# Optimization experiments

Measured on AMD Instinct MI355X. Metric: run time of the kernel, lower is better.

## Reference

```python
import jax, jax.numpy as jnp
import numpy as np

D_MODEL = 768
NUM_HEADS = 12
D_K = D_MODEL // NUM_HEADS
SCALE = float(np.sqrt(D_K))


def setup_inputs() -> dict:
    key = jax.random.key(0)
    ks = jax.random.split(key, 9)
    B, S, D = 2, 2048, D_MODEL
    std = 1.0 / np.sqrt(D)
    x = jax.random.normal(ks[0], (B, S, D), dtype=jnp.float32)
    attention_mask = jnp.ones((B, S), dtype=jnp.int32)
    # Linear params: weight [out, in] (torch convention), bias [out]
    Wq = jax.random.normal(ks[1], (D, D), dtype=jnp.float32) * std
    bq = jax.random.normal(ks[2], (D,), dtype=jnp.float32) * 0.01
    Wk = jax.random.normal(ks[3], (D, D), dtype=jnp.float32) * std
    bk = jax.random.normal(ks[4], (D,), dtype=jnp.float32) * 0.01
    Wv = jax.random.normal(ks[5], (D, D), dtype=jnp.float32) * std
    bv = jax.random.normal(ks[6], (D,), dtype=jnp.float32) * 0.01
    Wo = jax.random.normal(ks[7], (D, D), dtype=jnp.float32) * std
    bo = jax.random.normal(ks[8], (D,), dtype=jnp.float32) * 0.01
    return {"x": x, "attention_mask": attention_mask,
            "Wq": Wq, "bq": bq, "Wk": Wk, "bk": bk,
            "Wv": Wv, "bv": bv, "Wo": Wo, "bo": bo}


def reference(x, attention_mask, Wq, bq, Wk, bk, Wv, bv, Wo, bo):
    B, S, D = x.shape
    H, Dk = NUM_HEADS, D_K
    # QKV projections (torch Linear: x @ W.T + b)
    q = (x @ Wq.T + bq).reshape(B, S, H, Dk).transpose(0, 2, 1, 3)  # [B,H,S,Dk]
    k = (x @ Wk.T + bk).reshape(B, S, H, Dk).transpose(0, 2, 1, 3)
    v = (x @ Wv.T + bv).reshape(B, S, H, Dk).transpose(0, 2, 1, 3)
    scores = jnp.einsum('bhqd,bhkd->bhqk', q, k) / SCALE  # [B,H,S,S]
    mask = attention_mask[:, None, None, :]  # [B,1,1,S]
    scores = jnp.where(mask == 0, jnp.float32(-jnp.inf), scores)
    attn = jax.nn.softmax(scores, axis=-1)
    # dropout is identity in eval mode
    ctx = jnp.einsum('bhqk,bhkd->bhqd', attn, v)  # [B,H,S,Dk]
    ctx = ctx.transpose(0, 2, 1, 3).reshape(B, S, D)
    return ctx @ Wo.T + bo
```

## Files before the change

### kernel.cpp

```cpp
#include <hip/hip_runtime.h>
#include <stdint.h>

#define NHEAD 12
#define DKH   64
#define BB    2
#define SS    2048
#define DMOD  768
#define MTOT  (BB*SS)
#define NCHUNK 2
#define CHS   (SS/NCHUNK)
#define QBLK  128
#define NT    (CHS/64)

typedef __attribute__((ext_vector_type(8)))  _Float16 half8;
typedef __attribute__((ext_vector_type(4)))  _Float16 half4;
typedef __attribute__((ext_vector_type(2)))  __fp16   fp16x2;
typedef __attribute__((ext_vector_type(4)))  float    f32x4;
typedef __attribute__((ext_vector_type(16))) float    f32x16;

typedef __attribute__((address_space(1))) const void gv_t;
typedef __attribute__((address_space(3))) void       lv_t;

__device__ inline float fexp2(float x) { return __builtin_amdgcn_exp2f(x); }
__device__ inline int pk2(float a, float b) {
    union { fp16x2 h; int i; } u;
    u.h = __builtin_amdgcn_cvt_pkrtz(a, b);
    return u.i;
}

__global__ void k_cvtall(const float* __restrict__ x,
                         const float* __restrict__ w0, const float* __restrict__ w1,
                         const float* __restrict__ w2, const float* __restrict__ w3,
                         _Float16* __restrict__ xb,
                         _Float16* __restrict__ o0, _Float16* __restrict__ o1,
                         _Float16* __restrict__ o2, _Float16* __restrict__ o3) {
    const float* in; _Float16* out; int base;
    int blk = blockIdx.x;
    if (blk < 3072)      { in = x;  out = xb; base = blk; }
    else if (blk < 3648) { in = w0; out = o0; base = blk - 3072; }
    else if (blk < 4224) { in = w1; out = o1; base = blk - 3648; }
    else if (blk < 4800) { in = w2; out = o2; base = blk - 4224; }
    else                 { in = w3; out = o3; base = blk - 4800; }
    int i = (base * 256 + threadIdx.x) * 4;
    float4 v = *(const float4*)(in + i);
    half4 o;
    o.x = (_Float16)v.x; o.y = (_Float16)v.y; o.z = (_Float16)v.z; o.w = (_Float16)v.w;
    *(half4*)(out + i) = o;
}

template<int MODE>
__global__ __launch_bounds__(256, 2) void k_gemm(
    const _Float16* __restrict__ A, const _Float16* __restrict__ Bm,
    const float* __restrict__ bias0, const float* __restrict__ bias1, const float* __restrict__ bias2,
    float* __restrict__ outF,
    _Float16* __restrict__ Qd, _Float16* __restrict__ Kd, _Float16* __restrict__ Vtd,
    int K, int Ncols)
{
    __shared__ _Float16 As[128 * 64];
    __shared__ _Float16 Bs[128 * 64];
    const int tid = threadIdx.x;
    const int w = tid >> 6, l = tid & 63, lr = l & 15, lg = l >> 4;
    const int bm = blockIdx.y * 128, bn = blockIdx.x * 128;
    const int wm = (w >> 1) * 64, wn = (w & 1) * 64;
    f32x4 acc[4][4] = {};

    for (int k0 = 0; k0 < K; k0 += 64) {
        __syncthreads();
#pragma unroll
        for (int i = 0; i < 4; ++i) {
            int o  = w * 4096 + i * 1024 + l * 16;
            int lo = o ^ (((o >> 7) & 7) << 4);
            int row = lo >> 7;
            int colb = lo & 127;
            __builtin_amdgcn_global_load_lds(
                (gv_t*)((const char*)A + ((size_t)(bm + row) * K + k0) * 2 + colb),
                (lv_t*)((char*)As + w * 4096 + i * 1024), 16, 0, 0);
            __builtin_amdgcn_global_load_lds(
                (gv_t*)((const char*)Bm + ((size_t)(bn + row) * K + k0) * 2 + colb),
                (lv_t*)((char*)Bs + w * 4096 + i * 1024), 16, 0, 0);
        }
        __syncthreads();
#pragma unroll
        for (int kk = 0; kk < 2; ++kk) {
            half8 af[4], bf[4];
#pragma unroll
            for (int f = 0; f < 4; ++f) {
                int ob = ((wm + f * 16 + lr) * 128 + kk * 64 + lg * 16) ^ ((lr & 7) << 4);
                af[f] = *(const half8*)((const char*)As + ob);
                int ob2 = ((wn + f * 16 + lr) * 128 + kk * 64 + lg * 16) ^ ((lr & 7) << 4);
                bf[f] = *(const half8*)((const char*)Bs + ob2);
            }
            __builtin_amdgcn_s_setprio(1);
#pragma unroll
            for (int fm = 0; fm < 4; ++fm)
#pragma unroll
                for (int fn = 0; fn < 4; ++fn)
                    acc[fm][fn] = __builtin_amdgcn_mfma_f32_16x16x32_f16(af[fm], bf[fn], acc[fm][fn], 0, 0, 0);
            __builtin_amdgcn_s_setprio(0);
        }
    }

#pragma unroll
    for (int fm = 0; fm < 4; ++fm) {
#pragma unroll
        for (int fn = 0; fn < 4; ++fn) {
            int n = bn + wn + fn * 16 + lr;
            if (MODE == 0) {
                float bia = bias0[n];
#pragma unroll
                for (int j = 0; j < 4; ++j) {
                    int m = bm + wm + fm * 16 + lg * 4 + j;
                    outF[(size_t)m * Ncols + n] = acc[fm][fn][j] + bia;
                }
            } else {
                int qkv = n / 768, nn = n - qkv * 768;
                const float* bp = (qkv == 0) ? bias0 : (qkv == 1 ? bias1 : bias2);
                float bia = bp[nn];
                int h = nn >> 6, dk = nn & 63;
                int m0 = bm + wm + fm * 16 + lg * 4;
                int b = m0 >> 11;
                int s0 = m0 & 2047;
                size_t head = (size_t)b * NHEAD + h;
                if (qkv == 2) {
                    half4 pk;
#pragma unroll
                    for (int j = 0; j < 4; ++j) pk[j] = (_Float16)(acc[fm][fn][j] + bia);
                    *(half4*)(Vtd + (head * DKH + dk) * SS + s0) = pk;
                } else {
                    _Float16* dst = (qkv == 0) ? Qd : Kd;
                    float qsc = (qkv == 0) ? 0.18033688011f : 1.0f;
#pragma unroll
                    for (int j = 0; j < 4; ++j)
                        dst[(head * SS + (s0 + j)) * DKH + dk] = (_Float16)((acc[fm][fn][j] + bia) * qsc);
                }
            }
        }
    }
}

__global__ __launch_bounds__(256, 3) void k_attn(
    const _Float16* __restrict__ Qd, const _Float16* __restrict__ Kd,
    const _Float16* __restrict__ Vtd, const int* __restrict__ mask,
    _Float16* __restrict__ Opart, float* __restrict__ Mpart, float* __restrict__ Lpart)
{
    __shared__ _Float16 Ks[2 * 64 * 64];
    __shared__ _Float16 Vs[2 * 64 * 64];
    const int tid = threadIdx.x, w = tid >> 6, l = tid & 63;
    const int lq = l & 31, lhi = l >> 5;
    const int head  = blockIdx.x;
    const int qt    = blockIdx.y;
    const int chunk = blockIdx.z;
    const int b = head / NHEAD;
    const char* Qh = (const char*)(Qd + (size_t)head * SS * DKH);
    const char* Kh = (const char*)(Kd + (size_t)head * SS * DKH) + (size_t)chunk * CHS * 128;
    const char* Vh = (const char*)(Vtd + (size_t)head * DKH * SS);
    const int vcb = chunk * CHS * 2;

    const int q = qt * QBLK + w * 32 + lq;
    half8 qf[4];
#pragma unroll
    for (int kd = 0; kd < 4; ++kd)
        qf[kd] = *(const half8*)(Qh + ((size_t)q * 64 + kd * 16 + lhi * 8) * 2);

    f32x16 accO[2] = {};
    float m = -__builtin_inff(), lsum = 0.f;

    auto STAGE = [&](int kt2, int buf) {
#pragma unroll
        for (int i = 0; i < 2; ++i) {
            int o  = w * 2048 + i * 1024 + l * 16;
            int lo = o ^ (((o >> 7) & 7) << 4);
            __builtin_amdgcn_global_load_lds(
                (gv_t*)(Kh + (size_t)kt2 * 8192 + lo),
                (lv_t*)((char*)Ks + buf * 8192 + w * 2048 + i * 1024), 16, 0, 0);
            int dv = lo >> 7, inner = lo & 127;
            __builtin_amdgcn_global_load_lds(
                (gv_t*)(Vh + (size_t)dv * 4096 + vcb + kt2 * 128 + inner),
                (lv_t*)((char*)Vs + buf * 8192 + w * 2048 + i * 1024), 16, 0, 0);
        }
    };

    STAGE(0, 0);
    int cur = 0;

    for (int kt = 0; kt < NT; ++kt) {
        __syncthreads();
        if (kt < NT - 1) STAGE(kt + 1, cur ^ 1);
        int mv = mask[b * SS + chunk * CHS + kt * 64 + l];
        unsigned long long bal = __ballot(mv != 0);
        const char* kb = (const char*)Ks + cur * 8192;
        const char* vb = (const char*)Vs + cur * 8192;

        f32x16 s0 = {}, s1 = {};
#pragma unroll
        for (int kd = 0; kd < 4; ++kd) {
            int col = kd * 32 + lhi * 16;
            int ob0 = (lq * 128 + col) ^ ((lq & 7) << 4);
            half8 kf0 = *(const half8*)(kb + ob0);
            s0 = __builtin_amdgcn_mfma_f32_32x32x16_f16(kf0, qf[kd], s0, 0, 0, 0);
            int ob1 = ((32 + lq) * 128 + col) ^ ((lq & 7) << 4);
            half8 kf1 = *(const half8*)(kb + ob1);
            s1 = __builtin_amdgcn_mfma_f32_32x32x16_f16(kf1, qf[kd], s1, 0, 0, 0);
        }

        if (bal != ~0ull) {
#pragma unroll
            for (int r = 0; r < 16; ++r) {
                int kv0 = (r & 3) + 8 * (r >> 2) + 4 * lhi;
                if (!((bal >> kv0) & 1))        s0[r] = -__builtin_inff();
                if (!((bal >> (kv0 + 32)) & 1)) s1[r] = -__builtin_inff();
            }
        }

        float t[16];
#pragma unroll
        for (int i = 0; i < 16; ++i) t[i] = fmaxf(s0[i], s1[i]);
#pragma unroll
        for (int i = 0; i < 8; ++i) t[i] = fmaxf(t[i], t[i + 8]);
#pragma unroll
        for (int i = 0; i < 4; ++i) t[i] = fmaxf(t[i], t[i + 4]);
        t[0] = fmaxf(fmaxf(t[0], t[2]), fmaxf(t[1], t[3]));
        float pmax = fmaxf(t[0], __shfl_xor(t[0], 32, 64));

        if (!__all(pmax <= m + 3.0f)) {
            float mnew = fmaxf(m, pmax);
            float f = fexp2(m - mnew);
            m = mnew; lsum *= f;
            accO[0] *= f; accO[1] *= f;
        }
        float mex = fmaxf(m, -1e30f);

#pragma unroll
        for (int i = 0; i < 16; ++i) { s0[i] = fexp2(s0[i] - mex); s1[i] = fexp2(s1[i] - mex); }
#pragma unroll
        for (int i = 0; i < 16; ++i) t[i] = s0[i] + s1[i];
#pragma unroll
        for (int i = 0; i < 8; ++i) t[i] = t[i] + t[i + 8];
#pragma unroll
        for (int i = 0; i < 4; ++i) t[i] = t[i] + t[i + 4];
        t[0] = (t[0] + t[2]) + (t[1] + t[3]);
        lsum += t[0] + __shfl_xor(t[0], 32, 64);

        union PF { int w[4]; half8 h; } pf[4];
        {
            int W[8];
#pragma unroll
            for (int mm = 0; mm < 8; ++mm) W[mm] = pk2(s0[2 * mm], s0[2 * mm + 1]);
            asm("v_permlane32_swap_b32 %0, %1" : "+v"(W[0]), "+v"(W[2]));
            asm("v_permlane32_swap_b32 %0, %1" : "+v"(W[1]), "+v"(W[3]));
            asm("v_permlane32_swap_b32 %0, %1" : "+v"(W[4]), "+v"(W[6]));
            asm("v_permlane32_swap_b32 %0, %1" : "+v"(W[5]), "+v"(W[7]));
            pf[0].w[0] = W[0]; pf[0].w[1] = W[1]; pf[0].w[2] = W[2]; pf[0].w[3] = W[3];
            pf[1].w[0] = W[4]; pf[1].w[1] = W[5]; pf[1].w[2] = W[6]; pf[1].w[3] = W[7];
#pragma unroll
            for (int mm = 0; mm < 8; ++mm) W[mm] = pk2(s1[2 * mm], s1[2 * mm + 1]);
            asm("v_permlane32_swap_b32 %0, %1" : "+v"(W[0]), "+v"(W[2]));
            asm("v_permlane32_swap_b32 %0, %1" : "+v"(W[1]), "+v"(W[3]));
            asm("v_permlane32_swap_b32 %0, %1" : "+v"(W[4]), "+v"(W[6]));
            asm("v_permlane32_swap_b32 %0, %1" : "+v"(W[5]), "+v"(W[7]));
            pf[2].w[0] = W[0]; pf[2].w[1] = W[1]; pf[2].w[2] = W[2]; pf[2].w[3] = W[3];
            pf[3].w[0] = W[4]; pf[3].w[1] = W[5]; pf[3].w[2] = W[6]; pf[3].w[3] = W[7];
        }

#pragma unroll
        for (int cc = 0; cc < 4; ++cc) {
            int col = cc * 32 + lhi * 16;
#pragma unroll
            for (int ds = 0; ds < 2; ++ds) {
                int vrow = ds * 32 + lq;
                int ob = (vrow * 128 + col) ^ ((lq & 7) << 4);
                half8 vf = *(const half8*)(vb + ob);
                accO[ds] = __builtin_amdgcn_mfma_f32_32x32x16_f16(vf, pf[cc].h, accO[ds], 0, 0, 0);
            }
        }
        cur ^= 1;
    }

    const size_t prow = (size_t)(chunk * BB * NHEAD + head) * SS;
    if (lhi == 0) { Mpart[prow + q] = m; Lpart[prow + q] = lsum; }
#pragma unroll
    for (int ds = 0; ds < 2; ++ds)
#pragma unroll
        for (int rq = 0; rq < 4; ++rq) {
            half4 hv;
#pragma unroll
            for (int j = 0; j < 4; ++j) hv[j] = (_Float16)accO[ds][rq * 4 + j];
            *(half4*)(Opart + (prow + q) * DKH + ds * 32 + rq * 8 + lhi * 4) = hv;
        }
}

__global__ __launch_bounds__(256) void k_merge(
    const _Float16* __restrict__ Opart, const float* __restrict__ Mpart,
    const float* __restrict__ Lpart, _Float16* __restrict__ Ctx)
{
    int row  = blockIdx.x * 4 + (threadIdx.x >> 6);
    int lane = threadIdx.x & 63;
    int head = row >> 11, q = row & 2047;
    int b = head / NHEAD, h = head - b * NHEAD;
    float m[NCHUNK], lv[NCHUNK], M = -__builtin_inff();
#pragma unroll
    for (int c = 0; c < NCHUNK; ++c) {
        size_t pr = (size_t)(c * BB * NHEAD + head) * SS + q;
        m[c] = Mpart[pr]; lv[c] = Lpart[pr];
        M = fmaxf(M, m[c]);
    }
    float outv = 0.f;
    if (M > -1e37f) {
        float L = 0.f, acc = 0.f;
#pragma unroll
        for (int c = 0; c < NCHUNK; ++c) {
            float wgt = fexp2(m[c] - M);
            L += lv[c] * wgt;
            acc += wgt * (float)Opart[((size_t)(c * BB * NHEAD + head) * SS + q) * DKH + lane];
        }
        outv = acc / L;
    }
    Ctx[((size_t)(b * SS) + q) * DMOD + h * DKH + lane] = (_Float16)outv;
}

extern "C" void kernel_launch(void* const* d_in, const int* in_sizes, int n_in,
                              void* d_out, int out_size, void* d_ws, size_t ws_size,
                              hipStream_t stream) {
    const float* x  = (const float*)d_in[0];
    const int*  msk = (const int*)d_in[1];
    const float* Wq = (const float*)d_in[2];
    const float* bq = (const float*)d_in[3];
    const float* Wk = (const float*)d_in[4];
    const float* bk = (const float*)d_in[5];
    const float* Wv = (const float*)d_in[6];
    const float* bv = (const float*)d_in[7];
    const float* Wo = (const float*)d_in[8];
    const float* bo = (const float*)d_in[9];

    char* ws = (char*)d_ws;
    _Float16* Xb   = (_Float16*)(ws);
    _Float16* Wqkv = (_Float16*)(ws + 6291456);
    _Float16* Wob  = (_Float16*)(ws + 9830400);
    _Float16* Qd   = (_Float16*)(ws + 11010048);
    _Float16* Kd   = (_Float16*)(ws + 17301504);
    _Float16* Vtd  = (_Float16*)(ws + 23592960);
    _Float16* Ctxb = (_Float16*)(ws + 29884416);
    _Float16* Opart= (_Float16*)(ws + 36175872);
    float*    Mpart= (float*)   (ws + 48758784);
    float*    Lpart= (float*)   (ws + 49152000);

    k_cvtall<<<5376, 256, 0, stream>>>(x, Wq, Wk, Wv, Wo,
                                       Xb, Wqkv, Wqkv + 589824, Wqkv + 1179648, Wob);

    k_gemm<1><<<dim3(18, 32), 256, 0, stream>>>(Xb, Wqkv, bq, bk, bv,
                                                nullptr, Qd, Kd, Vtd, DMOD, 0);
    k_attn<<<dim3(24, 16, NCHUNK), 256, 0, stream>>>(Qd, Kd, Vtd, msk, Opart, Mpart, Lpart);
    k_merge<<<12288, 256, 0, stream>>>(Opart, Mpart, Lpart, Ctxb);
    k_gemm<0><<<dim3(6, 32), 256, 0, stream>>>(Ctxb, Wob, bo, nullptr, nullptr,
                                               (float*)d_out, nullptr, nullptr, nullptr,
                                               DMOD, DMOD);
}
```

Before: 106.0 us.

## Fuse split-softmax merge into output projection GEMM A-tile load

Removes the separate merge kernel and its Ctx buffer round trip. The output-projection GEMM now builds its A tile directly from the two partial attention outputs and their max/sum statistics, combining and normalizing them in registers before writing to LDS. This saves a launch and a global write and read of the context tensor. The cost is that each of the 6 column blocks redoes the merge for its rows, and the A loads become synchronous register loads instead of async global-to-LDS copies. The QKV GEMM is also de-templated, with the LDS destination offset written as the per-lane offset.

Measured after the change: 118.8 us. 1.12x slower.

```diff
diff --git a/kernel.cpp b/kernel.cpp
--- a/kernel.cpp
+++ b/kernel.cpp
@@ -48,13 +48,10 @@
     *(half4*)(out + i) = o;
 }
 
-template<int MODE>
-__global__ __launch_bounds__(256, 2) void k_gemm(
+__global__ __launch_bounds__(256, 2) void k_gemm_qkv(
     const _Float16* __restrict__ A, const _Float16* __restrict__ Bm,
     const float* __restrict__ bias0, const float* __restrict__ bias1, const float* __restrict__ bias2,
-    float* __restrict__ outF,
-    _Float16* __restrict__ Qd, _Float16* __restrict__ Kd, _Float16* __restrict__ Vtd,
-    int K, int Ncols)
+    _Float16* __restrict__ Qd, _Float16* __restrict__ Kd, _Float16* __restrict__ Vtd)
 {
     __shared__ _Float16 As[128 * 64];
     __shared__ _Float16 Bs[128 * 64];
@@ -62,6 +59,7 @@
     const int w = tid >> 6, l = tid & 63, lr = l & 15, lg = l >> 4;
     const int bm = blockIdx.y * 128, bn = blockIdx.x * 128;
     const int wm = (w >> 1) * 64, wn = (w & 1) * 64;
+    const int K = DMOD;
     f32x4 acc[4][4] = {};
 
     for (int k0 = 0; k0 < K; k0 += 64) {
@@ -74,10 +72,10 @@
             int colb = lo & 127;
             __builtin_amdgcn_global_load_lds(
                 (gv_t*)((const char*)A + ((size_t)(bm + row) * K + k0) * 2 + colb),
-                (lv_t*)((char*)As + w * 4096 + i * 1024), 16, 0, 0);
+                (lv_t*)((char*)As + o), 16, 0, 0);
             __builtin_amdgcn_global_load_lds(
                 (gv_t*)((const char*)Bm + ((size_t)(bn + row) * K + k0) * 2 + colb),
-                (lv_t*)((char*)Bs + w * 4096 + i * 1024), 16, 0, 0);
+                (lv_t*)((char*)Bs + o), 16, 0, 0);
         }
         __syncthreads();
 #pragma unroll
@@ -105,34 +103,109 @@
 #pragma unroll
         for (int fn = 0; fn < 4; ++fn) {
             int n = bn + wn + fn * 16 + lr;
-            if (MODE == 0) {
-                float bia = bias0[n];
-#pragma unroll
-                for (int j = 0; j < 4; ++j) {
-                    int m = bm + wm + fm * 16 + lg * 4 + j;
-                    outF[(size_t)m * Ncols + n] = acc[fm][fn][j] + bia;
-                }
+            int qkv = n / 768, nn = n - qkv * 768;
+            const float* bp = (qkv == 0) ? bias0 : (qkv == 1 ? bias1 : bias2);
+            float bia = bp[nn];
+            int h = nn >> 6, dk = nn & 63;
+            int m0 = bm + wm + fm * 16 + lg * 4;
+            int b = m0 >> 11;
+            int s0 = m0 & 2047;
+            size_t head = (size_t)b * NHEAD + h;
+            if (qkv == 2) {
+                half4 pk;
+#pragma unroll
+                for (int j = 0; j < 4; ++j) pk[j] = (_Float16)(acc[fm][fn][j] + bia);
+                *(half4*)(Vtd + (head * DKH + dk) * SS + s0) = pk;
             } else {
-                int qkv = n / 768, nn = n - qkv * 768;
-                const float* bp = (qkv == 0) ? bias0 : (qkv == 1 ? bias1 : bias2);
-                float bia = bp[nn];
-                int h = nn >> 6, dk = nn & 63;
-                int m0 = bm + wm + fm * 16 + lg * 4;
-                int b = m0 >> 11;
-                int s0 = m0 & 2047;
-                size_t head = (size_t)b * NHEAD + h;
-                if (qkv == 2) {
-                    half4 pk;
-#pragma unroll
-                    for (int j = 0; j < 4; ++j) pk[j] = (_Float16)(acc[fm][fn][j] + bia);
-                    *(half4*)(Vtd + (head * DKH + dk) * SS + s0) = pk;
-                } else {
-                    _Float16* dst = (qkv == 0) ? Qd : Kd;
-                    float qsc = (qkv == 0) ? 0.18033688011f : 1.0f;
-#pragma unroll
-                    for (int j = 0; j < 4; ++j)
-                        dst[(head * SS + (s0 + j)) * DKH + dk] = (_Float16)((acc[fm][fn][j] + bia) * qsc);
-                }
+                _Float16* dst = (qkv == 0) ? Qd : Kd;
+                float qsc = (qkv == 0) ? 0.18033688011f : 1.0f;
+#pragma unroll
+                for (int j = 0; j < 4; ++j)
+                    dst[(head * SS + (s0 + j)) * DKH + dk] = (_Float16)((acc[fm][fn][j] + bia) * qsc);
+            }
+        }
+    }
+}
+
+__global__ __launch_bounds__(256, 2) void k_proj(
+    const _Float16* __restrict__ Opart, const float* __restrict__ Mpart,
+    const float* __restrict__ Lpart, const _Float16* __restrict__ Wob,
+    const float* __restrict__ bo, float* __restrict__ outF)
+{
+    __shared__ _Float16 As[128 * 64];
+    __shared__ _Float16 Bs[128 * 64];
+    const int tid = threadIdx.x;
+    const int w = tid >> 6, l = tid & 63, lr = l & 15, lg = l >> 4;
+    const int bm = blockIdx.y * 128, bn = blockIdx.x * 128;
+    const int wm = (w >> 1) * 64, wn = (w & 1) * 64;
+    const int K = DMOD;
+    f32x4 acc[4][4] = {};
+
+    for (int k0 = 0; k0 < K; k0 += 64) {
+        __syncthreads();
+#pragma unroll
+        for (int i = 0; i < 4; ++i) {
+            int o  = w * 4096 + i * 1024 + l * 16;
+            int lo = o ^ (((o >> 7) & 7) << 4);
+            int row = lo >> 7;
+            int colb = lo & 127;
+            __builtin_amdgcn_global_load_lds(
+                (gv_t*)((const char*)Wob + ((size_t)(bn + row) * K + k0) * 2 + colb),
+                (lv_t*)((char*)Bs + o), 16, 0, 0);
+            int mrow = bm + row;
+            int k = k0 + (colb >> 1);
+            int h = k >> 6, dv = k & 63;
+            int b = mrow >> 11, s = mrow & 2047;
+            size_t r0 = (size_t)(b * NHEAD + h) * SS + s;
+            size_t r1 = r0 + (size_t)BB * NHEAD * SS;
+            half8 p0 = *(const half8*)(Opart + r0 * DKH + dv);
+            half8 p1 = *(const half8*)(Opart + r1 * DKH + dv);
+            float m0 = Mpart[r0], m1 = Mpart[r1];
+            float l0 = Lpart[r0], l1 = Lpart[r1];
+            float M = fmaxf(m0, m1);
+            float w0 = 0.f, w1 = 0.f;
+            if (M > -1e37f) {
+                w0 = fexp2(m0 - M); w1 = fexp2(m1 - M);
+                float inv = 1.0f / (l0 * w0 + l1 * w1);
+                w0 *= inv; w1 *= inv;
+            }
+            half8 res;
+#pragma unroll
+            for (int j = 0; j < 8; ++j)
+                res[j] = (_Float16)((float)p0[j] * w0 + (float)p1[j] * w1);
+            *(half8*)((char*)As + o) = res;
+        }
+        __syncthreads();
+#pragma unroll
+        for (int kk = 0; kk < 2; ++kk) {
+            half8 af[4], bf[4];
+#pragma unroll
+            for (int f = 0; f < 4; ++f) {
+                int ob = ((wm + f * 16 + lr) * 128 + kk * 64 + lg * 16) ^ ((lr & 7) << 4);
+                af[f] = *(const half8*)((const char*)As + ob);
+                int ob2 = ((wn + f * 16 + lr) * 128 + kk * 64 + lg * 16) ^ ((lr & 7) << 4);
+                bf[f] = *(const half8*)((const char*)Bs + ob2);
+            }
+            __builtin_amdgcn_s_setprio(1);
+#pragma unroll
+            for (int fm = 0; fm < 4; ++fm)
+#pragma unroll
+                for (int fn = 0; fn < 4; ++fn)
+                    acc[fm][fn] = __builtin_amdgcn_mfma_f32_16x16x32_f16(af[fm], bf[fn], acc[fm][fn], 0, 0, 0);
+            __builtin_amdgcn_s_setprio(0);
+        }
+    }
+
+#pragma unroll
+    for (int fm = 0; fm < 4; ++fm) {
+#pragma unroll
+        for (int fn = 0; fn < 4; ++fn) {
+            int n = bn + wn + fn * 16 + lr;
+            float bia = bo[n];
+#pragma unroll
+            for (int j = 0; j < 4; ++j) {
+                int m = bm + wm + fm * 16 + lg * 4 + j;
+                outF[(size_t)m * DMOD + n] = acc[fm][fn][j] + bia;
             }
         }
     }
@@ -289,35 +362,6 @@
         }
 }
 
-__global__ __launch_bounds__(256) void k_merge(
-    const _Float16* __restrict__ Opart, const float* __restrict__ Mpart,
-    const float* __restrict__ Lpart, _Float16* __restrict__ Ctx)
-{
-    int row  = blockIdx.x * 4 + (threadIdx.x >> 6);
-    int lane = threadIdx.x & 63;
-    int head = row >> 11, q = row & 2047;
-    int b = head / NHEAD, h = head - b * NHEAD;
-    float m[NCHUNK], lv[NCHUNK], M = -__builtin_inff();
-#pragma unroll
-    for (int c = 0; c < NCHUNK; ++c) {
-        size_t pr = (size_t)(c * BB * NHEAD + head) * SS + q;
-        m[c] = Mpart[pr]; lv[c] = Lpart[pr];
-        M = fmaxf(M, m[c]);
-    }
-    float outv = 0.f;
-    if (M > -1e37f) {
-        float L = 0.f, acc = 0.f;
-#pragma unroll
-        for (int c = 0; c < NCHUNK; ++c) {
-            float wgt = fexp2(m[c] - M);
-            L += lv[c] * wgt;
-            acc += wgt * (float)Opart[((size_t)(c * BB * NHEAD + head) * SS + q) * DKH + lane];
-        }
-        outv = acc / L;
-    }
-    Ctx[((size_t)(b * SS) + q) * DMOD + h * DKH + lane] = (_Float16)outv;
-}
-
 extern "C" void kernel_launch(void* const* d_in, const int* in_sizes, int n_in,
                               void* d_out, int out_size, void* d_ws, size_t ws_size,
                               hipStream_t stream) {
@@ -339,7 +383,6 @@
     _Float16* Qd   = (_Float16*)(ws + 11010048);
     _Float16* Kd   = (_Float16*)(ws + 17301504);
     _Float16* Vtd  = (_Float16*)(ws + 23592960);
-    _Float16* Ctxb = (_Float16*)(ws + 29884416);
     _Float16* Opart= (_Float16*)(ws + 36175872);
     float*    Mpart= (float*)   (ws + 48758784);
     float*    Lpart= (float*)   (ws + 49152000);
@@ -347,11 +390,7 @@
     k_cvtall<<<5376, 256, 0, stream>>>(x, Wq, Wk, Wv, Wo,
                                        Xb, Wqkv, Wqkv + 589824, Wqkv + 1179648, Wob);
 
-    k_gemm<1><<<dim3(18, 32), 256, 0, stream>>>(Xb, Wqkv, bq, bk, bv,
-                                                nullptr, Qd, Kd, Vtd, DMOD, 0);
+    k_gemm_qkv<<<dim3(18, 32), 256, 0, stream>>>(Xb, Wqkv, bq, bk, bv, Qd, Kd, Vtd);
     k_attn<<<dim3(24, 16, NCHUNK), 256, 0, stream>>>(Qd, Kd, Vtd, msk, Opart, Mpart, Lpart);
-    k_merge<<<12288, 256, 0, stream>>>(Opart, Mpart, Lpart, Ctxb);
-    k_gemm<0><<<dim3(6, 32), 256, 0, stream>>>(Ctxb, Wob, bo, nullptr, nullptr,
-                                               (float*)d_out, nullptr, nullptr, nullptr,
-                                               DMOD, DMOD);
-}
+    k_proj<<<dim3(6, 32), 256, 0, stream>>>(Opart, Mpart, Lpart, Wob, bo, (float*)d_out);
+}
```
